# Optimization experiments

Hardware: AMD Instinct MI355X
Metric: run time of the kernel (lower is better)

Reference implementation:

```python
import jax, jax.numpy as jnp
import numpy as np

DIM = 768
H = 12
D = DIM // H            # 64
SCALE = D ** -0.5
M = 64                  # landmarks for pnp heads
PINV_ITERS = 6
PNP_HEADS = 11          # heads 0..10 use Nystrom, head 11 uses softmax


def setup_inputs() -> dict:
    key = jax.random.key(0)
    ks = jax.random.split(key, 5)
    B, N = 4, 4096
    x = jax.random.normal(ks[0], (B, N, DIM), jnp.float32)
    qkv_w = jax.random.normal(ks[1], (3 * DIM, DIM), jnp.float32) * (DIM ** -0.5)
    qkv_b = jax.random.normal(ks[2], (3 * DIM,), jnp.float32) * 0.01
    proj_w = jax.random.normal(ks[3], (DIM, DIM), jnp.float32) * (DIM ** -0.5)
    proj_b = jax.random.normal(ks[4], (DIM,), jnp.float32) * 0.01
    return {"x": x, "qkv_w": qkv_w, "qkv_b": qkv_b, "proj_w": proj_w, "proj_b": proj_b}


def moore_penrose_iter_pinv(x, iters=PINV_ITERS):
    # x: [B, h, M, M]. Original torch code takes torch.max over the whole per-head
    # tensor (incl. batch), so normalize with a per-head scalar over axes (B, M).
    abs_x = jnp.abs(x)
    col_max = abs_x.sum(axis=-1, keepdims=True).max(axis=(0, 2, 3), keepdims=True)
    row_max = abs_x.sum(axis=-2, keepdims=True).max(axis=(0, 2, 3), keepdims=True)
    z = jnp.swapaxes(x, -1, -2) / (col_max * row_max)
    I = jnp.eye(x.shape[-1], dtype=x.dtype)
    for _ in range(iters):
        xz = x @ z
        z = 0.25 * (z @ (13.0 * I - xz @ (15.0 * I - xz @ (7.0 * I - xz))))
    return z


def reference(x, qkv_w, qkv_b, proj_w, proj_b):
    B, N, C = x.shape
    qkv = (x @ qkv_w.T + qkv_b).reshape(B, N, 3, H, D).transpose(2, 0, 3, 1, 4)  # [3,B,H,N,D]
    q, k, v = qkv[0] * SCALE, qkv[1], qkv[2]

    # ---- Nystrom (pnp) heads 0..PNP_HEADS-1, all with the same M -> vectorized ----
    qp, kp, vp = q[:, :PNP_HEADS], k[:, :PNP_HEADS], v[:, :PNP_HEADS]
    idxs = jnp.array([int(i * N / M) for i in range(M)], dtype=jnp.int32)
    q_m = qp[:, :, idxs, :]   # [B,h,M,D] landmark queries
    k_m = kp[:, :, idxs, :]   # [B,h,M,D] landmark keys

    SA = jnp.einsum('bhnd,bhmd->bhnm', qp, k_m)   # [B,h,N,M]
    SC = jnp.einsum('bhmd,bhnd->bhmn', q_m, kp)   # [B,h,M,N]
    SB = jnp.einsum('bhmd,bhld->bhml', q_m, k_m)  # [B,h,M,M]

    eA = jnp.exp(SA - SA.max(axis=-1, keepdims=True))
    sc_max = SC.max(axis=-1, keepdims=True)       # [B,h,M,1]
    eC = jnp.exp(SC - sc_max)
    eB = jnp.exp(jnp.clip(SB - sc_max, -88.0, None))

    v_aug = jnp.concatenate([vp, jnp.ones_like(vp[..., :1])], axis=-1)  # [B,h,N,D+1]
    pi = moore_penrose_iter_pinv(eB)
    prod = (eA @ pi) @ (eC @ v_aug)               # [B,h,N,D+1]
    out_p = prod[..., :-1] / jnp.maximum(prod[..., -1:], 1e-8)

    # ---- fallback softmax head(s) ----
    qs, ks_, vs = q[:, PNP_HEADS:], k[:, PNP_HEADS:], v[:, PNP_HEADS:]
    attn = jax.nn.softmax(jnp.einsum('bhnd,bhmd->bhnm', qs, ks_), axis=-1)
    out_s = attn @ vs

    ctx = jnp.concatenate([out_p, out_s], axis=1).transpose(0, 2, 1, 3).reshape(B, N, C)
    return ctx @ proj_w.T + proj_b
```

## Files before the change

kernel.cpp:

```cpp
#include <hip/hip_runtime.h>


typedef __attribute__((ext_vector_type(8))) short short8;
typedef __attribute__((ext_vector_type(4))) float f32x4;
typedef __attribute__((ext_vector_type(4))) unsigned short ushort4v;

static __device__ __forceinline__ unsigned short f2bf(float f) {
    union { float f; unsigned u; } x; x.f = f;
    unsigned r = x.u + 0x7fffu + ((x.u >> 16) & 1u);
    return (unsigned short)(r >> 16);
}

static __device__ __forceinline__ float b2f(unsigned short u) {
    union { unsigned u; float f; } t; t.u = (unsigned)u << 16; return t.f;
}

static __device__ __forceinline__ void bfsplit(float x, unsigned short& h, unsigned short& l) {
    unsigned short hh = f2bf(x);
    union { unsigned u; float f; } t; t.u = (unsigned)hh << 16;
    h = hh;
    l = f2bf(x - t.f);
}

__global__ __launch_bounds__(256) void preconv(
    const float* __restrict__ in, unsigned short* __restrict__ hi,
    unsigned short* __restrict__ lo, int n4)
{
    for (int i = blockIdx.x * 256 + threadIdx.x; i < n4; i += gridDim.x * 256) {
        float4 f = *(const float4*)(in + (size_t)i * 4);
        float vs[4] = {f.x, f.y, f.z, f.w};
        ushort4v h, l;
        #pragma unroll
        for (int j = 0; j < 4; ++j) {
            unsigned short hh, ll;
            bfsplit(vs[j], hh, ll);
            h[j] = hh; l[j] = ll;
        }
        *(ushort4v*)(hi + (size_t)i * 4) = h;
        *(ushort4v*)(lo + (size_t)i * 4) = l;
    }
}

__global__ __launch_bounds__(256, 2) void gemm_qk_mfma(
    const unsigned short* __restrict__ Xh, const unsigned short* __restrict__ Xl,
    const unsigned short* __restrict__ Wh, const unsigned short* __restrict__ Wl,
    const float* __restrict__ bias,
    unsigned short* __restrict__ qh, unsigned short* __restrict__ ql,
    unsigned short* __restrict__ kh, unsigned short* __restrict__ kl)
{
    __shared__ unsigned short Ah[4096], Al[4096], Bh[4096], Bl[4096];
    const int tid = threadIdx.x;
    const int bid = blockIdx.x;
    const int swz = (bid & 7) * 192 + (bid >> 3);
    const int brow = (swz / 12) << 7, bcol = (swz % 12) << 7;
    const int ln = tid & 63, wv = tid >> 6;
    const int wr = (wv >> 1) << 6, wc = (wv & 1) << 6;
    const int srow = tid >> 1, sc = (tid & 1) << 1;
    const size_t ag = (size_t)(brow + srow) * 768 + (sc << 3);
    const size_t bg = (size_t)(bcol + srow) * 768 + (sc << 3);
    const int fr = ln & 15, fc = ln >> 4;
    const int i0 = srow * 32 + (((sc + 0) ^ (srow & 3)) << 3);
    const int i1 = srow * 32 + (((sc + 1) ^ (srow & 3)) << 3);

    f32x4 acc[4][4] = {};
    for (int k0 = 0; k0 < 768; k0 += 32) {
        short8 xh0 = *(const short8*)(Xh + ag + k0);
        short8 xh1 = *(const short8*)(Xh + ag + k0 + 8);
        short8 xl0 = *(const short8*)(Xl + ag + k0);
        short8 xl1 = *(const short8*)(Xl + ag + k0 + 8);
        short8 wh0 = *(const short8*)(Wh + bg + k0);
        short8 wh1 = *(const short8*)(Wh + bg + k0 + 8);
        short8 wl0 = *(const short8*)(Wl + bg + k0);
        short8 wl1 = *(const short8*)(Wl + bg + k0 + 8);
        __syncthreads();
        *(short8*)&Ah[i0] = xh0; *(short8*)&Ah[i1] = xh1;
        *(short8*)&Al[i0] = xl0; *(short8*)&Al[i1] = xl1;
        *(short8*)&Bh[i0] = wh0; *(short8*)&Bh[i1] = wh1;
        *(short8*)&Bl[i0] = wl0; *(short8*)&Bl[i1] = wl1;
        __syncthreads();
        short8 ah[4], al[4], bh[4], bl[4];
        #pragma unroll
        for (int i = 0; i < 4; ++i) {
            int ar = wr + (i << 4) + fr;
            int aidx = ar * 32 + ((fc ^ (ar & 3)) << 3);
            ah[i] = *(short8*)&Ah[aidx];
            al[i] = *(short8*)&Al[aidx];
            int br2 = wc + (i << 4) + fr;
            int bidx = br2 * 32 + ((fc ^ (br2 & 3)) << 3);
            bh[i] = *(short8*)&Bh[bidx];
            bl[i] = *(short8*)&Bl[bidx];
        }
        #pragma unroll
        for (int i = 0; i < 4; ++i)
            #pragma unroll
            for (int j = 0; j < 4; ++j) {
                acc[i][j] = __builtin_amdgcn_mfma_f32_16x16x32_bf16(ah[i], bh[j], acc[i][j], 0, 0, 0);
                acc[i][j] = __builtin_amdgcn_mfma_f32_16x16x32_bf16(ah[i], bl[j], acc[i][j], 0, 0, 0);
                acc[i][j] = __builtin_amdgcn_mfma_f32_16x16x32_bf16(al[i], bh[j], acc[i][j], 0, 0, 0);
            }
    }
    const int fg = ln >> 4;
    #pragma unroll
    for (int j = 0; j < 4; ++j) {
        int c = bcol + wc + (j << 4) + fr;
        float bb = bias[c];
        int isk = c >> 9 >= 1 ? (c >= 768) : 0;
        int rem = c - (c >= 768 ? 768 : 0);
        int h = rem >> 6, d = rem & 63;
        #pragma unroll
        for (int i = 0; i < 4; ++i)
            #pragma unroll
            for (int r = 0; r < 4; ++r) {
                int row = brow + wr + (i << 4) + (fg << 2) + r;
                int b = row >> 12, n = row & 4095;
                float val = acc[i][j][r] + bb;
                size_t idx = (((size_t)(b * 12 + h) << 12) + n) * 64 + d;
                unsigned short hh, ll;
                if (c < 768) {
                    bfsplit(val * 0.125f, hh, ll);
                    qh[idx] = hh; ql[idx] = ll;
                } else {
                    bfsplit(val, hh, ll);
                    kh[idx] = hh; kl[idx] = ll;
                }
            }
        (void)isk;
    }
}

__global__ __launch_bounds__(256, 2) void gemm_v_mfma(
    const unsigned short* __restrict__ Xh, const unsigned short* __restrict__ Wh,
    const float* __restrict__ bias, unsigned short* __restrict__ vh)
{
    __shared__ unsigned short Ah[4096], Bh[4096];
    const int tid = threadIdx.x;
    const int bid = blockIdx.x;
    const int swz = (bid & 7) * 96 + (bid >> 3);
    const int brow = (swz / 6) << 7, bcol = 1536 + ((swz % 6) << 7);
    const int ln = tid & 63, wv = tid >> 6;
    const int wr = (wv >> 1) << 6, wc = (wv & 1) << 6;
    const int srow = tid >> 1, sc = (tid & 1) << 1;
    const size_t ag = (size_t)(brow + srow) * 768 + (sc << 3);
    const size_t bg = (size_t)(bcol + srow) * 768 + (sc << 3);
    const int fr = ln & 15, fc = ln >> 4;
    const int i0 = srow * 32 + (((sc + 0) ^ (srow & 3)) << 3);
    const int i1 = srow * 32 + (((sc + 1) ^ (srow & 3)) << 3);

    f32x4 acc[4][4] = {};
    for (int k0 = 0; k0 < 768; k0 += 32) {
        short8 xh0 = *(const short8*)(Xh + ag + k0);
        short8 xh1 = *(const short8*)(Xh + ag + k0 + 8);
        short8 wh0 = *(const short8*)(Wh + bg + k0);
        short8 wh1 = *(const short8*)(Wh + bg + k0 + 8);
        __syncthreads();
        *(short8*)&Ah[i0] = xh0; *(short8*)&Ah[i1] = xh1;
        *(short8*)&Bh[i0] = wh0; *(short8*)&Bh[i1] = wh1;
        __syncthreads();
        short8 ah[4], bh[4];
        #pragma unroll
        for (int i = 0; i < 4; ++i) {
            int ar = wr + (i << 4) + fr;
            ah[i] = *(short8*)&Ah[ar * 32 + ((fc ^ (ar & 3)) << 3)];
            int br2 = wc + (i << 4) + fr;
            bh[i] = *(short8*)&Bh[br2 * 32 + ((fc ^ (br2 & 3)) << 3)];
        }
        #pragma unroll
        for (int i = 0; i < 4; ++i)
            #pragma unroll
            for (int j = 0; j < 4; ++j)
                acc[i][j] = __builtin_amdgcn_mfma_f32_16x16x32_bf16(ah[i], bh[j], acc[i][j], 0, 0, 0);
    }
    const int fg = ln >> 4;
    #pragma unroll
    for (int j = 0; j < 4; ++j) {
        int c = bcol + wc + (j << 4) + fr;
        float bb = bias[c];
        int rem = c - 1536;
        int h = rem >> 6, d = rem & 63;
        #pragma unroll
        for (int i = 0; i < 4; ++i)
            #pragma unroll
            for (int r = 0; r < 4; ++r) {
                int row = brow + wr + (i << 4) + (fg << 2) + r;
                int b = row >> 12, n = row & 4095;
                float val = acc[i][j][r] + bb;
                size_t idx = (((size_t)(b * 12 + h) << 12) + n) * 64 + d;
                vh[idx] = f2bf(val);
            }
    }
}

__global__ __launch_bounds__(256) void wflash(
    const unsigned short* __restrict__ qh, const unsigned short* __restrict__ ql,
    const unsigned short* __restrict__ khg, const unsigned short* __restrict__ klg,
    const unsigned short* __restrict__ vhg,
    float* __restrict__ wacc, float* __restrict__ wl, float* __restrict__ wm)
{
    int chunk = blockIdx.x;
    int bh = blockIdx.y;
    int b = bh / 11, h = bh - b * 11;
    size_t base = ((size_t)(b * 12 + h)) << 12;
    __shared__ unsigned short kh_s[64][72], kl_s[64][72];
    __shared__ unsigned short vth[64][72];
    __shared__ unsigned short ph[4][16][72], pl[4][16][72];
    int tid = threadIdx.x;
    int wv = tid >> 6, ln = tid & 63;
    int rr = tid >> 2, dg = (tid & 3) << 4;
    const int arow = (wv << 4) + (ln & 15);
    const int ak0 = (ln >> 4) << 3;
    const int rg = (ln >> 4) << 2;
    short8 aqh0, aql0, aqh1, aql1;
    {
        size_t off = ((base + ((size_t)arow << 6)) << 6) + ak0;
        aqh0 = *(const short8*)(qh + off);
        aqh1 = *(const short8*)(qh + off + 32);
        aql0 = *(const short8*)(ql + off);
        aql1 = *(const short8*)(ql + off + 32);
    }
    f32x4 o_acc[4] = {};
    float mr[4] = {-1e30f, -1e30f, -1e30f, -1e30f};
    float lr[4] = {};
    for (int t = 0; t < 8; ++t) {
        int n0 = (chunk << 9) + (t << 6);
        __syncthreads();
        {
            size_t off = ((base + n0 + rr) << 6) + dg;
            *(short8*)&kh_s[rr][dg]     = *(const short8*)(khg + off);
            *(short8*)&kh_s[rr][dg + 8] = *(const short8*)(khg + off + 8);
            *(short8*)&kl_s[rr][dg]     = *(const short8*)(klg + off);
            *(short8*)&kl_s[rr][dg + 8] = *(const short8*)(klg + off + 8);
            short8 v0 = *(const short8*)(vhg + off);
            short8 v1 = *(const short8*)(vhg + off + 8);
            #pragma unroll
            for (int i = 0; i < 8; ++i) {
                vth[dg + i][rr]     = (unsigned short)v0[i];
                vth[dg + 8 + i][rr] = (unsigned short)v1[i];
            }
        }
        __syncthreads();
        f32x4 s_acc[4];
        #pragma unroll
        for (int jb = 0; jb < 4; ++jb) {
            f32x4 z = {};
            const int brow2 = (jb << 4) + (ln & 15);
            short8 bh0 = *(short8*)&kh_s[brow2][ak0];
            short8 bh1 = *(short8*)&kh_s[brow2][ak0 + 32];
            short8 bl0 = *(short8*)&kl_s[brow2][ak0];
            short8 bl1 = *(short8*)&kl_s[brow2][ak0 + 32];
            z = __builtin_amdgcn_mfma_f32_16x16x32_bf16(aqh0, bh0, z, 0, 0, 0);
            z = __builtin_amdgcn_mfma_f32_16x16x32_bf16(aqh0, bl0, z, 0, 0, 0);
            z = __builtin_amdgcn_mfma_f32_16x16x32_bf16(aql0, bh0, z, 0, 0, 0);
            z = __builtin_amdgcn_mfma_f32_16x16x32_bf16(aqh1, bh1, z, 0, 0, 0);
            z = __builtin_amdgcn_mfma_f32_16x16x32_bf16(aqh1, bl1, z, 0, 0, 0);
            z = __builtin_amdgcn_mfma_f32_16x16x32_bf16(aql1, bh1, z, 0, 0, 0);
            s_acc[jb] = z;
        }
        float mx[4];
        #pragma unroll
        for (int r = 0; r < 4; ++r)
            mx[r] = fmaxf(fmaxf(s_acc[0][r], s_acc[1][r]),
                          fmaxf(s_acc[2][r], s_acc[3][r]));
        #pragma unroll
        for (int off2 = 1; off2 < 16; off2 <<= 1)
            #pragma unroll
            for (int r = 0; r < 4; ++r)
                mx[r] = fmaxf(mx[r], __shfl_xor(mx[r], off2, 64));
        float fac[4];
        #pragma unroll
        for (int r = 0; r < 4; ++r) {
            float mn = fmaxf(mr[r], mx[r]);
            fac[r] = expf(mr[r] - mn);
            mr[r] = mn;
        }
        float rs[4] = {};
        #pragma unroll
        for (int jb = 0; jb < 4; ++jb)
            #pragma unroll
            for (int r = 0; r < 4; ++r) {
                float p = expf(s_acc[jb][r] - mr[r]);
                rs[r] += p;
                unsigned short hh, ll;
                bfsplit(p, hh, ll);
                ph[wv][rg + r][(jb << 4) + (ln & 15)] = hh;
                pl[wv][rg + r][(jb << 4) + (ln & 15)] = ll;
            }
        #pragma unroll
        for (int off2 = 1; off2 < 16; off2 <<= 1)
            #pragma unroll
            for (int r = 0; r < 4; ++r)
                rs[r] += __shfl_xor(rs[r], off2, 64);
        #pragma unroll
        for (int r = 0; r < 4; ++r) lr[r] = lr[r] * fac[r] + rs[r];
        #pragma unroll
        for (int jb = 0; jb < 4; ++jb)
            #pragma unroll
            for (int r = 0; r < 4; ++r)
                o_acc[jb][r] *= fac[r];
        short8 pah0 = *(short8*)&ph[wv][ln & 15][ak0];
        short8 pah1 = *(short8*)&ph[wv][ln & 15][ak0 + 32];
        short8 pal0 = *(short8*)&pl[wv][ln & 15][ak0];
        short8 pal1 = *(short8*)&pl[wv][ln & 15][ak0 + 32];
        #pragma unroll
        for (int jb = 0; jb < 4; ++jb) {
            const int brow2 = (jb << 4) + (ln & 15);
            short8 bv0 = *(short8*)&vth[brow2][ak0];
            short8 bv1 = *(short8*)&vth[brow2][ak0 + 32];
            f32x4 o = o_acc[jb];
            o = __builtin_amdgcn_mfma_f32_16x16x32_bf16(pah0, bv0, o, 0, 0, 0);
            o = __builtin_amdgcn_mfma_f32_16x16x32_bf16(pal0, bv0, o, 0, 0, 0);
            o = __builtin_amdgcn_mfma_f32_16x16x32_bf16(pah1, bv1, o, 0, 0, 0);
            o = __builtin_amdgcn_mfma_f32_16x16x32_bf16(pal1, bv1, o, 0, 0, 0);
            o_acc[jb] = o;
        }
    }
    int cidx = (bh << 3) + chunk;
    #pragma unroll
    for (int jb = 0; jb < 4; ++jb)
        #pragma unroll
        for (int r = 0; r < 4; ++r) {
            int row = (wv << 4) + rg + r, col = (jb << 4) + (ln & 15);
            wacc[((size_t)cidx << 12) + ((size_t)row << 6) + col] = o_acc[jb][r];
        }
    if ((ln & 15) == 0)
        #pragma unroll
        for (int r = 0; r < 4; ++r) {
            int row = (wv << 4) + rg + r;
            wl[cidx * 64 + row] = lr[r];
            wm[cidx * 64 + row] = mr[r];
        }
}

__global__ __launch_bounds__(256) void wmerge(
    const float* __restrict__ wacc, const float* __restrict__ wl,
    const float* __restrict__ wm,
    float* __restrict__ Wb, float* __restrict__ scm)
{
    int bh = blockIdx.x;
    int tid = threadIdx.x;
    __shared__ float fcs[8][64];
    if (tid < 64) {
        float mx = -1e30f;
        #pragma unroll
        for (int c = 0; c < 8; ++c)
            mx = fmaxf(mx, wm[((bh << 3) + c) * 64 + tid]);
        scm[(bh << 6) + tid] = mx;
        #pragma unroll
        for (int c = 0; c < 8; ++c)
            fcs[c][tid] = expf(wm[((bh << 3) + c) * 64 + tid] - mx);
    }
    __syncthreads();
    for (int e = tid; e < 4096; e += 256) {
        int m = e >> 6, j = e & 63;
        float s = 0.f;
        #pragma unroll
        for (int c = 0; c < 8; ++c)
            s += fcs[c][m] * wacc[((size_t)((bh << 3) + c) << 12) + e];
        Wb[(size_t)bh * 4160 + m * 65 + j] = s;
    }
    if (tid < 64) {
        float s = 0.f;
        #pragma unroll
        for (int c = 0; c < 8; ++c)
            s += fcs[c][tid] * wl[((bh << 3) + c) * 64 + tid];
        Wb[(size_t)bh * 4160 + tid * 65 + 64] = s;
    }
}

__global__ __launch_bounds__(256) void eb_kernel(
    const unsigned short* __restrict__ qh, const unsigned short* __restrict__ ql,
    const unsigned short* __restrict__ kh, const unsigned short* __restrict__ kl,
    const float* __restrict__ scm, float* __restrict__ eB)
{
    int bh = blockIdx.x;
    int b = bh / 11, h = bh - b * 11;
    size_t base = ((size_t)(b * 12 + h)) << 12;
    __shared__ float qm[64][65], km[64][65];
    int tid = threadIdx.x;
    for (int e = tid; e < 4096; e += 256) {
        int mm = e >> 6, d = e & 63;
        size_t off = ((base + ((size_t)mm << 6)) << 6) + d;
        qm[mm][d] = b2f(qh[off]) + b2f(ql[off]);
        km[mm][d] = b2f(kh[off]) + b2f(kl[off]);
    }
    __syncthreads();
    int m = tid >> 2, l0 = tid & 3;
    float smax = scm[(bh << 6) + m];
    for (int l = l0; l < 64; l += 4) {
        float s = 0.f;
        #pragma unroll
        for (int d = 0; d < 64; ++d) s += qm[m][d] * km[l][d];
        eB[((size_t)bh << 12) + (m << 6) + l] = expf(fmaxf(s - smax, -88.f));
    }
}

__global__ __launch_bounds__(256) void norms_kernel(
    const float* __restrict__ eB, float* __restrict__ denom)
{
    int h = blockIdx.x;
    int tid = threadIdx.x;
    int b = tid >> 6, idx = tid & 63;
    int bh = b * 11 + h;
    const float* E = eB + ((size_t)bh << 12);
    float rs = 0.f, cs = 0.f;
    #pragma unroll 4
    for (int l = 0; l < 64; ++l) rs += E[(idx << 6) + l];
    #pragma unroll 4
    for (int m = 0; m < 64; ++m) cs += E[(m << 6) + idx];
    __shared__ float r1[256], r2[256];
    r1[tid] = rs; r2[tid] = cs;
    __syncthreads();
    for (int s = 128; s > 0; s >>= 1) {
        if (tid < s) {
            r1[tid] = fmaxf(r1[tid], r1[tid + s]);
            r2[tid] = fmaxf(r2[tid], r2[tid + s]);
        }
        __syncthreads();
    }
    if (tid == 0) denom[h] = r1[0] * r2[0];
}

__device__ __forceinline__ void mm64x3(
    const unsigned short (&Ahi)[64][72], const unsigned short (&Alo)[64][72],
    const unsigned short (&BThi)[64][72], const unsigned short (&BTlo)[64][72],
    int wr, int wc, int fr, int fk, f32x4 (&acc)[2][2])
{
    #pragma unroll
    for (int ks = 0; ks < 2; ++ks) {
        const int kb = (ks << 5) + fk;
        short8 ah[2], al[2], bh[2], bl[2];
        #pragma unroll
        for (int i = 0; i < 2; ++i) {
            ah[i] = *(const short8*)&Ahi[wr + (i << 4) + fr][kb];
            al[i] = *(const short8*)&Alo[wr + (i << 4) + fr][kb];
            bh[i] = *(const short8*)&BThi[wc + (i << 4) + fr][kb];
            bl[i] = *(const short8*)&BTlo[wc + (i << 4) + fr][kb];
        }
        #pragma unroll
        for (int i = 0; i < 2; ++i)
            #pragma unroll
            for (int j = 0; j < 2; ++j) {
                acc[i][j] = __builtin_amdgcn_mfma_f32_16x16x32_bf16(ah[i], bh[j], acc[i][j], 0, 0, 0);
                acc[i][j] = __builtin_amdgcn_mfma_f32_16x16x32_bf16(ah[i], bl[j], acc[i][j], 0, 0, 0);
                acc[i][j] = __builtin_amdgcn_mfma_f32_16x16x32_bf16(al[i], bh[j], acc[i][j], 0, 0, 0);
            }
    }
}

__global__ __launch_bounds__(256) void pinv_kernel(
    const float* __restrict__ eB, const float* __restrict__ denom,
    float* __restrict__ pi_)
{
    __shared__ unsigned short Xh[64][72],  Xl[64][72];
    __shared__ unsigned short Zh[64][72],  Zl[64][72];
    __shared__ unsigned short ZTh[64][72], ZTl[64][72];
    __shared__ unsigned short Mh[64][72],  Ml[64][72];
    __shared__ unsigned short MTh[64][72], MTl[64][72];
    __shared__ unsigned short Th[64][72],  Tbl[64][72];
    __shared__ float Zf[64][68];
    int bh = blockIdx.x;
    int h = bh % 11;
    int tid = threadIdx.x;
    float dn = denom[h];
    const int ln = tid & 63, wv = tid >> 6;
    const int wr = (wv >> 1) << 5, wc = (wv & 1) << 5;
    const int fr = ln & 15, fk = (ln >> 4) << 3;
    const int rg = (ln >> 4) << 2;

    for (int e = tid; e < 4096; e += 256) {
        int m = e >> 6, l = e & 63;
        float xv = eB[((size_t)bh << 12) + e];
        unsigned short hh, ll;
        bfsplit(xv, hh, ll);
        Xh[m][l] = hh; Xl[m][l] = ll;
        float zv = xv / dn;
        Zf[l][m] = zv;
        bfsplit(zv, hh, ll);
        Zh[l][m] = hh; Zl[l][m] = ll;
        ZTh[m][l] = hh; ZTl[m][l] = ll;
    }
    __syncthreads();

    for (int it = 0; it < 6; ++it) {
        f32x4 mm1[2][2] = {};
        mm64x3(Xh, Xl, ZTh, ZTl, wr, wc, fr, fk, mm1);
        #pragma unroll
        for (int i = 0; i < 2; ++i)
            #pragma unroll
            for (int j = 0; j < 2; ++j)
                #pragma unroll
                for (int r = 0; r < 4; ++r) {
                    int row = wr + (i << 4) + rg + r, col = wc + (j << 4) + fr;
                    unsigned short hh, ll;
                    bfsplit(mm1[i][j][r], hh, ll);
                    Mh[row][col] = hh;  Ml[row][col] = ll;
                    MTh[col][row] = hh; MTl[col][row] = ll;
                }
        __syncthreads();
        f32x4 a2[2][2] = {};
        mm64x3(Mh, Ml, MTh, MTl, wr, wc, fr, fk, a2);
        #pragma unroll
        for (int i = 0; i < 2; ++i)
            #pragma unroll
            for (int j = 0; j < 2; ++j)
                #pragma unroll
                for (int r = 0; r < 4; ++r) {
                    int row = wr + (i << 4) + rg + r, col = wc + (j << 4) + fr;
                    float val = 7.f * mm1[i][j][r] - a2[i][j][r];
                    unsigned short hh, ll;
                    bfsplit(val, hh, ll);
                    Th[col][row] = hh; Tbl[col][row] = ll;
                }
        __syncthreads();
        f32x4 a3[2][2] = {};
        mm64x3(Mh, Ml, Th, Tbl, wr, wc, fr, fk, a3);
        __syncthreads();
        #pragma unroll
        for (int i = 0; i < 2; ++i)
            #pragma unroll
            for (int j = 0; j < 2; ++j)
                #pragma unroll
                for (int r = 0; r < 4; ++r) {
                    int row = wr + (i << 4) + rg + r, col = wc + (j << 4) + fr;
                    float val = 15.f * mm1[i][j][r] - a3[i][j][r];
                    unsigned short hh, ll;
                    bfsplit(val, hh, ll);
                    Th[col][row] = hh; Tbl[col][row] = ll;
                }
        __syncthreads();
        f32x4 a4[2][2] = {};
        mm64x3(Zh, Zl, Th, Tbl, wr, wc, fr, fk, a4);
        float zn[2][2][4];
        #pragma unroll
        for (int i = 0; i < 2; ++i)
            #pragma unroll
            for (int j = 0; j < 2; ++j)
                #pragma unroll
                for (int r = 0; r < 4; ++r) {
                    int row = wr + (i << 4) + rg + r, col = wc + (j << 4) + fr;
                    zn[i][j][r] = 0.25f * (13.f * Zf[row][col] - a4[i][j][r]);
                }
        __syncthreads();
        #pragma unroll
        for (int i = 0; i < 2; ++i)
            #pragma unroll
            for (int j = 0; j < 2; ++j)
                #pragma unroll
                for (int r = 0; r < 4; ++r) {
                    int row = wr + (i << 4) + rg + r, col = wc + (j << 4) + fr;
                    float val = zn[i][j][r];
                    Zf[row][col] = val;
                    unsigned short hh, ll;
                    bfsplit(val, hh, ll);
                    Zh[row][col] = hh;  Zl[row][col] = ll;
                    ZTh[col][row] = hh; ZTl[col][row] = ll;
                }
        __syncthreads();
    }
    for (int e = tid; e < 4096; e += 256)
        pi_[((size_t)bh << 12) + e] = Zf[e >> 6][e & 63];
}

__global__ __launch_bounds__(256) void pw_kernel(
    const float* __restrict__ pi_, const float* __restrict__ Wb,
    float* __restrict__ Tb)
{
    int bh = blockIdx.x;
    __shared__ float P[64][65];
    __shared__ float Wl[64][66];
    int tid = threadIdx.x;
    for (int e = tid; e < 4096; e += 256)
        P[e >> 6][e & 63] = pi_[((size_t)bh << 12) + e];
    for (int e = tid; e < 64 * 65; e += 256) {
        int l = e / 65, j = e - l * 65;
        Wl[l][j] = Wb[(size_t)bh * 4160 + e];
    }
    __syncthreads();
    int m = tid & 63, g = tid >> 6;
    #pragma unroll
    for (int t = 0; t < 17; ++t) {
        int j = g + (t << 2);
        if (j > 64) break;
        float s = 0.f;
        #pragma unroll
        for (int l = 0; l < 64; ++l) s += P[m][l] * Wl[l][j];
        Tb[(size_t)((bh << 6) + m) * 65 + j] = s;
    }
}

__global__ __launch_bounds__(256) void outp_kernel(
    const unsigned short* __restrict__ qh, const unsigned short* __restrict__ ql,
    const unsigned short* __restrict__ khg, const unsigned short* __restrict__ klg,
    const float* __restrict__ Tb, unsigned short* __restrict__ ctxh)
{
    int bh = blockIdx.y;
    int b = bh / 11, h = bh - b * 11;
    int n0 = blockIdx.x << 6;
    size_t base = ((size_t)(b * 12 + h)) << 12;
    __shared__ unsigned short kmh[64][72], kml[64][72];
    __shared__ unsigned short tth[64][72], ttl[64][72];
    __shared__ unsigned short ph[4][16][72], pl[4][16][72];
    __shared__ float t64[64];
    int tid = threadIdx.x;
    int wv = tid >> 6, ln = tid & 63;
    int rr = tid >> 2, dg = (tid & 3) << 4;
    const int arow = (wv << 4) + (ln & 15);
    const int ak0 = (ln >> 4) << 3;
    const int rg = (ln >> 4) << 2;
    {
        size_t off = ((base + ((size_t)rr << 6)) << 6) + dg;
        *(short8*)&kmh[rr][dg]     = *(const short8*)(khg + off);
        *(short8*)&kmh[rr][dg + 8] = *(const short8*)(khg + off + 8);
        *(short8*)&kml[rr][dg]     = *(const short8*)(klg + off);
        *(short8*)&kml[rr][dg + 8] = *(const short8*)(klg + off + 8);
    }
    for (int e = tid; e < 4096; e += 256) {
        int m = e >> 6, j = e & 63;
        float tv = Tb[(size_t)((bh << 6) + m) * 65 + j];
        unsigned short hh, ll;
        bfsplit(tv, hh, ll);
        tth[j][m] = hh; ttl[j][m] = ll;
    }
    if (tid < 64) t64[tid] = Tb[(size_t)((bh << 6) + tid) * 65 + 64];
    short8 aqh0, aql0, aqh1, aql1;
    {
        size_t off = ((base + n0 + arow) << 6) + ak0;
        aqh0 = *(const short8*)(qh + off);
        aqh1 = *(const short8*)(qh + off + 32);
        aql0 = *(const short8*)(ql + off);
        aql1 = *(const short8*)(ql + off + 32);
    }
    __syncthreads();
    f32x4 s_acc[4];
    #pragma unroll
    for (int jb = 0; jb < 4; ++jb) {
        f32x4 z = {};
        const int brow2 = (jb << 4) + (ln & 15);
        short8 bh0 = *(short8*)&kmh[brow2][ak0];
        short8 bh1 = *(short8*)&kmh[brow2][ak0 + 32];
        short8 bl0 = *(short8*)&kml[brow2][ak0];
        short8 bl1 = *(short8*)&kml[brow2][ak0 + 32];
        z = __builtin_amdgcn_mfma_f32_16x16x32_bf16(aqh0, bh0, z, 0, 0, 0);
        z = __builtin_amdgcn_mfma_f32_16x16x32_bf16(aqh0, bl0, z, 0, 0, 0);
        z = __builtin_amdgcn_mfma_f32_16x16x32_bf16(aql0, bh0, z, 0, 0, 0);
        z = __builtin_amdgcn_mfma_f32_16x16x32_bf16(aqh1, bh1, z, 0, 0, 0);
        z = __builtin_amdgcn_mfma_f32_16x16x32_bf16(aqh1, bl1, z, 0, 0, 0);
        z = __builtin_amdgcn_mfma_f32_16x16x32_bf16(aql1, bh1, z, 0, 0, 0);
        s_acc[jb] = z;
    }
    float mx[4];
    #pragma unroll
    for (int r = 0; r < 4; ++r)
        mx[r] = fmaxf(fmaxf(s_acc[0][r], s_acc[1][r]),
                      fmaxf(s_acc[2][r], s_acc[3][r]));
    #pragma unroll
    for (int off2 = 1; off2 < 16; off2 <<= 1)
        #pragma unroll
        for (int r = 0; r < 4; ++r)
            mx[r] = fmaxf(mx[r], __shfl_xor(mx[r], off2, 64));
    float den[4] = {};
    #pragma unroll
    for (int jb = 0; jb < 4; ++jb) {
        float tj = t64[(jb << 4) + (ln & 15)];
        #pragma unroll
        for (int r = 0; r < 4; ++r) {
            float p = expf(s_acc[jb][r] - mx[r]);
            den[r] += p * tj;
            unsigned short hh, ll;
            bfsplit(p, hh, ll);
            ph[wv][rg + r][(jb << 4) + (ln & 15)] = hh;
            pl[wv][rg + r][(jb << 4) + (ln & 15)] = ll;
        }
    }
    #pragma unroll
    for (int off2 = 1; off2 < 16; off2 <<= 1)
        #pragma unroll
        for (int r = 0; r < 4; ++r)
            den[r] += __shfl_xor(den[r], off2, 64);
    short8 pah0 = *(short8*)&ph[wv][ln & 15][ak0];
    short8 pah1 = *(short8*)&ph[wv][ln & 15][ak0 + 32];
    short8 pal0 = *(short8*)&pl[wv][ln & 15][ak0];
    short8 pal1 = *(short8*)&pl[wv][ln & 15][ak0 + 32];
    f32x4 o_acc[4] = {};
    #pragma unroll
    for (int jb = 0; jb < 4; ++jb) {
        const int brow2 = (jb << 4) + (ln & 15);
        short8 bth0 = *(short8*)&tth[brow2][ak0];
        short8 bth1 = *(short8*)&tth[brow2][ak0 + 32];
        short8 btl0 = *(short8*)&ttl[brow2][ak0];
        short8 btl1 = *(short8*)&ttl[brow2][ak0 + 32];
        f32x4 o = o_acc[jb];
        o = __builtin_amdgcn_mfma_f32_16x16x32_bf16(pah0, bth0, o, 0, 0, 0);
        o = __builtin_amdgcn_mfma_f32_16x16x32_bf16(pah0, btl0, o, 0, 0, 0);
        o = __builtin_amdgcn_mfma_f32_16x16x32_bf16(pal0, bth0, o, 0, 0, 0);
        o = __builtin_amdgcn_mfma_f32_16x16x32_bf16(pah1, bth1, o, 0, 0, 0);
        o = __builtin_amdgcn_mfma_f32_16x16x32_bf16(pah1, btl1, o, 0, 0, 0);
        o = __builtin_amdgcn_mfma_f32_16x16x32_bf16(pal1, bth1, o, 0, 0, 0);
        o_acc[jb] = o;
    }
    float inv[4];
    #pragma unroll
    for (int r = 0; r < 4; ++r) inv[r] = 1.0f / fmaxf(den[r], 1e-8f);
    #pragma unroll
    for (int jb = 0; jb < 4; ++jb)
        #pragma unroll
        for (int r = 0; r < 4; ++r) {
            int row = n0 + (wv << 4) + rg + r;
            int col = (jb << 4) + (ln & 15);
            ctxh[((size_t)b * 4096 + row) * 768 + h * 64 + col] =
                f2bf(o_acc[jb][r] * inv[r]);
        }
}

__global__ __launch_bounds__(256) void flash_part(
    const unsigned short* __restrict__ qhg, const unsigned short* __restrict__ khg,
    const unsigned short* __restrict__ vhg,
    float* __restrict__ pacc, float* __restrict__ pm, float* __restrict__ pl)
{
    int bx = blockIdx.x, cy = blockIdx.y, b = blockIdx.z;
    int n0 = bx << 6;
    size_t base = ((size_t)(b * 12 + 11)) << 12;
    __shared__ unsigned short qs[64][72];
    __shared__ unsigned short ks[64][72];
    __shared__ unsigned short vts[64][72];
    __shared__ unsigned short ps[4][16][72];
    int tid = threadIdx.x;
    int wv = tid >> 6, ln = tid & 63;
    int rr = tid >> 2, dg = (tid & 3) << 4;
    {
        size_t off = ((base + n0 + rr) << 6) + dg;
        *(short8*)&qs[rr][dg]     = *(const short8*)(qhg + off);
        *(short8*)&qs[rr][dg + 8] = *(const short8*)(qhg + off + 8);
    }
    __syncthreads();
    const int arow = (wv << 4) + (ln & 15);
    const int ak0 = (ln >> 4) << 3;
    const int rg = (ln >> 4) << 2;
    short8 aq0 = *(short8*)&qs[arow][ak0];
    short8 aq1 = *(short8*)&qs[arow][ak0 + 32];
    f32x4 o_acc[4] = {};
    float mr[4] = {-1e30f, -1e30f, -1e30f, -1e30f};
    float lr[4] = {};
    for (int t = 0; t < 16; ++t) {
        int m0 = (cy << 10) + (t << 6);
        __syncthreads();
        {
            size_t off = ((base + m0 + rr) << 6) + dg;
            *(short8*)&ks[rr][dg]     = *(const short8*)(khg + off);
            *(short8*)&ks[rr][dg + 8] = *(const short8*)(khg + off + 8);
            short8 v0 = *(const short8*)(vhg + off);
            short8 v1 = *(const short8*)(vhg + off + 8);
            #pragma unroll
            for (int i = 0; i < 8; ++i) {
                vts[dg + i][rr]     = (unsigned short)v0[i];
                vts[dg + 8 + i][rr] = (unsigned short)v1[i];
            }
        }
        __syncthreads();
        f32x4 s_acc[4];
        #pragma unroll
        for (int jb = 0; jb < 4; ++jb) {
            f32x4 z = {};
            short8 bk0 = *(short8*)&ks[(jb << 4) + (ln & 15)][ak0];
            short8 bk1 = *(short8*)&ks[(jb << 4) + (ln & 15)][ak0 + 32];
            z = __builtin_amdgcn_mfma_f32_16x16x32_bf16(aq0, bk0, z, 0, 0, 0);
            z = __builtin_amdgcn_mfma_f32_16x16x32_bf16(aq1, bk1, z, 0, 0, 0);
            s_acc[jb] = z;
        }
        float mx[4];
        #pragma unroll
        for (int r = 0; r < 4; ++r)
            mx[r] = fmaxf(fmaxf(s_acc[0][r], s_acc[1][r]),
                          fmaxf(s_acc[2][r], s_acc[3][r]));
        #pragma unroll
        for (int off2 = 1; off2 < 16; off2 <<= 1)
            #pragma unroll
            for (int r = 0; r < 4; ++r)
                mx[r] = fmaxf(mx[r], __shfl_xor(mx[r], off2, 64));
        float fac[4];
        #pragma unroll
        for (int r = 0; r < 4; ++r) {
            float mn = fmaxf(mr[r], mx[r]);
            fac[r] = expf(mr[r] - mn);
            mr[r] = mn;
        }
        float rs[4] = {};
        #pragma unroll
        for (int jb = 0; jb < 4; ++jb)
            #pragma unroll
            for (int r = 0; r < 4; ++r) {
                float p = expf(s_acc[jb][r] - mr[r]);
                rs[r] += p;
                ps[wv][rg + r][(jb << 4) + (ln & 15)] = f2bf(p);
            }
        #pragma unroll
        for (int off2 = 1; off2 < 16; off2 <<= 1)
            #pragma unroll
            for (int r = 0; r < 4; ++r)
                rs[r] += __shfl_xor(rs[r], off2, 64);
        #pragma unroll
        for (int r = 0; r < 4; ++r) lr[r] = lr[r] * fac[r] + rs[r];
        #pragma unroll
        for (int jb = 0; jb < 4; ++jb)
            #pragma unroll
            for (int r = 0; r < 4; ++r)
                o_acc[jb][r] *= fac[r];
        short8 pa0 = *(short8*)&ps[wv][ln & 15][ak0];
        short8 pa1 = *(short8*)&ps[wv][ln & 15][ak0 + 32];
        #pragma unroll
        for (int jb = 0; jb < 4; ++jb) {
            short8 bv0 = *(short8*)&vts[(jb << 4) + (ln & 15)][ak0];
            short8 bv1 = *(short8*)&vts[(jb << 4) + (ln & 15)][ak0 + 32];
            f32x4 z = o_acc[jb];
            z = __builtin_amdgcn_mfma_f32_16x16x32_bf16(pa0, bv0, z, 0, 0, 0);
            z = __builtin_amdgcn_mfma_f32_16x16x32_bf16(pa1, bv1, z, 0, 0, 0);
            o_acc[jb] = z;
        }
    }
    int slot = (b * 4 + cy) * 64 + bx;
    #pragma unroll
    for (int jb = 0; jb < 4; ++jb)
        #pragma unroll
        for (int r = 0; r < 4; ++r) {
            int row = (wv << 4) + rg + r, col = (jb << 4) + (ln & 15);
            pacc[(size_t)slot * 4096 + (size_t)row * 64 + col] = o_acc[jb][r];
        }
    if ((ln & 15) == 0)
        #pragma unroll
        for (int r = 0; r < 4; ++r) {
            int row = (wv << 4) + rg + r;
            pm[(size_t)slot * 64 + row] = mr[r];
            pl[(size_t)slot * 64 + row] = lr[r];
        }
}

__global__ __launch_bounds__(256) void flash_merge(
    const float* __restrict__ pacc, const float* __restrict__ pm,
    const float* __restrict__ pl, unsigned short* __restrict__ ctxh)
{
    int bx = blockIdx.x, b = blockIdx.y;
    int tid = threadIdx.x, r = tid & 63, g = tid >> 6;
    float mc[4], mt = -1e30f;
    #pragma unroll
    for (int c = 0; c < 4; ++c) {
        mc[c] = pm[(size_t)((b * 4 + c) * 64 + bx) * 64 + r];
        mt = fmaxf(mt, mc[c]);
    }
    float fac[4], lt = 0.f;
    #pragma unroll
    for (int c = 0; c < 4; ++c) {
        fac[c] = expf(mc[c] - mt);
        lt += fac[c] * pl[(size_t)((b * 4 + c) * 64 + bx) * 64 + r];
    }
    float inv = 1.0f / lt;
    size_t obase = ((size_t)b * 4096 + (size_t)((bx << 6) + r)) * 768 + 11 * 64 + (g << 4);
    #pragma unroll
    for (int i = 0; i < 16; ++i) {
        float s = 0.f;
        #pragma unroll
        for (int c = 0; c < 4; ++c)
            s += fac[c] * pacc[(size_t)((b * 4 + c) * 64 + bx) * 4096 + (size_t)r * 64 + (g << 4) + i];
        ctxh[obase + i] = f2bf(s * inv);
    }
}

__global__ __launch_bounds__(256, 2) void gemm_proj_mfma(
    const unsigned short* __restrict__ Xh, const unsigned short* __restrict__ Wh,
    const float* __restrict__ bias, float* __restrict__ out)
{
    __shared__ unsigned short Ah[4096], Bh[4096];
    const int tid = threadIdx.x;
    const int bid = blockIdx.x;
    const int swz = (bid & 7) * 96 + (bid >> 3);
    const int brow = (swz / 6) << 7, bcol = (swz % 6) << 7;
    const int ln = tid & 63, wv = tid >> 6;
    const int wr = (wv >> 1) << 6, wc = (wv & 1) << 6;
    const int srow = tid >> 1, sc = (tid & 1) << 1;
    const size_t ag = (size_t)(brow + srow) * 768 + (sc << 3);
    const size_t bg = (size_t)(bcol + srow) * 768 + (sc << 3);
    const int fr = ln & 15, fc = ln >> 4;
    const int i0 = srow * 32 + (((sc + 0) ^ (srow & 3)) << 3);
    const int i1 = srow * 32 + (((sc + 1) ^ (srow & 3)) << 3);

    f32x4 acc[4][4] = {};
    for (int k0 = 0; k0 < 768; k0 += 32) {
        short8 xh0 = *(const short8*)(Xh + ag + k0);
        short8 xh1 = *(const short8*)(Xh + ag + k0 + 8);
        short8 wh0 = *(const short8*)(Wh + bg + k0);
        short8 wh1 = *(const short8*)(Wh + bg + k0 + 8);
        __syncthreads();
        *(short8*)&Ah[i0] = xh0; *(short8*)&Ah[i1] = xh1;
        *(short8*)&Bh[i0] = wh0; *(short8*)&Bh[i1] = wh1;
        __syncthreads();
        short8 ah[4], bh[4];
        #pragma unroll
        for (int i = 0; i < 4; ++i) {
            int ar = wr + (i << 4) + fr;
            ah[i] = *(short8*)&Ah[ar * 32 + ((fc ^ (ar & 3)) << 3)];
            int br2 = wc + (i << 4) + fr;
            bh[i] = *(short8*)&Bh[br2 * 32 + ((fc ^ (br2 & 3)) << 3)];
        }
        #pragma unroll
        for (int i = 0; i < 4; ++i)
            #pragma unroll
            for (int j = 0; j < 4; ++j)
                acc[i][j] = __builtin_amdgcn_mfma_f32_16x16x32_bf16(ah[i], bh[j], acc[i][j], 0, 0, 0);
    }
    const int fg = ln >> 4;
    #pragma unroll
    for (int j = 0; j < 4; ++j) {
        int c = bcol + wc + (j << 4) + fr;
        float bb = bias[c];
        #pragma unroll
        for (int i = 0; i < 4; ++i)
            #pragma unroll
            for (int r = 0; r < 4; ++r) {
                int row = brow + wr + (i << 4) + (fg << 2) + r;
                out[(size_t)row * 768 + c] = acc[i][j][r] + bb;
            }
    }
}

extern "C" void kernel_launch(void* const* d_in, const int* in_sizes, int n_in,
                              void* d_out, int out_size, void* d_ws, size_t ws_size,
                              hipStream_t stream)
{
    const float* x      = (const float*)d_in[0];
    const float* qkv_w  = (const float*)d_in[1];
    const float* qkv_b  = (const float*)d_in[2];
    const float* proj_w = (const float*)d_in[3];
    const float* proj_b = (const float*)d_in[4];
    float* out = (float*)d_out;

    const size_t QKV = (size_t)4 * 12 * 4096 * 64;
    unsigned short* qh = (unsigned short*)d_ws;
    unsigned short* ql = qh + QKV;
    unsigned short* kh = ql + QKV;
    unsigned short* kl = kh + QKV;
    unsigned short* vh = kl + QKV;
    unsigned short* ctxh = vh + QKV;
    float* scm  = (float*)(ctxh + QKV);
    float* eB   = scm + 4096;
    float* den  = eB + 44 * 4096;
    float* pi_  = den + 64;
    float* Wb   = pi_ + 44 * 4096;
    float* Tb   = Wb + 44 * 4160;
    unsigned short* Whi  = (unsigned short*)(Tb + 44 * 4160);
    unsigned short* Wlo  = Whi + (size_t)2304 * 768;
    unsigned short* Pwhi = Wlo + (size_t)2304 * 768;
    unsigned short* Pwlo = Pwhi + (size_t)768 * 768;

    unsigned short* Xhi = (unsigned short*)out;
    unsigned short* Xlo = Xhi + QKV;
    float* wacc = out;
    float* wl   = wacc + 1441792;
    float* wm   = wl + 22528;
    float* fpacc = out;
    float* fpm   = fpacc + 4194304;
    float* fpl   = fpm + 65536;

    preconv<<<2048, 256, 0, stream>>>(x, Xhi, Xlo, 3145728);
    preconv<<<1024, 256, 0, stream>>>(qkv_w, Whi, Wlo, 442368);
    preconv<<<512, 256, 0, stream>>>(proj_w, Pwhi, Pwlo, 147456);
    gemm_qk_mfma<<<1536, 256, 0, stream>>>(Xhi, Xlo, Whi, Wlo, qkv_b,
                                           qh, ql, kh, kl);
    gemm_v_mfma<<<768, 256, 0, stream>>>(Xhi, Whi, qkv_b, vh);
    wflash<<<dim3(8, 44), 256, 0, stream>>>(qh, ql, kh, kl, vh, wacc, wl, wm);
    wmerge<<<44, 256, 0, stream>>>(wacc, wl, wm, Wb, scm);
    eb_kernel<<<44, 256, 0, stream>>>(qh, ql, kh, kl, scm, eB);
    norms_kernel<<<11, 256, 0, stream>>>(eB, den);
    pinv_kernel<<<44, 256, 0, stream>>>(eB, den, pi_);
    pw_kernel<<<44, 256, 0, stream>>>(pi_, Wb, Tb);
    outp_kernel<<<dim3(64, 44), 256, 0, stream>>>(qh, ql, kh, kl, Tb, ctxh);
    flash_part<<<dim3(64, 4, 4), 256, 0, stream>>>(qh, kh, vh, fpacc, fpm, fpl);
    flash_merge<<<dim3(64, 4), 256, 0, stream>>>(fpacc, fpm, fpl, ctxh);
    gemm_proj_mfma<<<768, 256, 0, stream>>>(ctxh, Pwhi, proj_b, out);
}
```

Measured before the change: 456.3 us.

## Merge weight preconversion launches, deepen GEMM K-tiles, drop low-bf16 P terms

The three fp32-to-bf16 split launches become one kernel over a concatenated index range, which removes two launches. The V and projection GEMMs now stage 64-wide K tiles with an 8-way XOR swizzle, halving the number of barrier-separated iterations. The wflash and outp kernels no longer compute or use the low bf16 half of the softmax probabilities, which removes the shared-memory writes, loads and MFMAs for those terms. This lowers the precision of P in the Nystrom path, adding error that must stay within tolerance.

```diff
diff --git a/kernel.cpp b/kernel.cpp
--- a/kernel.cpp
+++ b/kernel.cpp
@@ -22,22 +22,31 @@
     l = f2bf(x - t.f);
 }
 
-__global__ __launch_bounds__(256) void preconv(
-    const float* __restrict__ in, unsigned short* __restrict__ hi,
-    unsigned short* __restrict__ lo, int n4)
-{
-    for (int i = blockIdx.x * 256 + threadIdx.x; i < n4; i += gridDim.x * 256) {
-        float4 f = *(const float4*)(in + (size_t)i * 4);
+__global__ __launch_bounds__(256) void preconv3(
+    const float* __restrict__ a, const float* __restrict__ b,
+    const float* __restrict__ c,
+    unsigned short* __restrict__ ahi, unsigned short* __restrict__ alo,
+    unsigned short* __restrict__ bhi, unsigned short* __restrict__ blo,
+    unsigned short* __restrict__ chi, unsigned short* __restrict__ clo)
+{
+    const int nA = 3145728, nB = 442368, nC = 147456;
+    const int total = nA + nB + nC;
+    for (int i = blockIdx.x * 256 + threadIdx.x; i < total; i += gridDim.x * 256) {
+        const float* src; unsigned short* hi; unsigned short* lo; int j;
+        if (i < nA)           { src = a; hi = ahi; lo = alo; j = i; }
+        else if (i < nA + nB) { src = b; hi = bhi; lo = blo; j = i - nA; }
+        else                  { src = c; hi = chi; lo = clo; j = i - nA - nB; }
+        float4 f = *(const float4*)(src + (size_t)j * 4);
         float vs[4] = {f.x, f.y, f.z, f.w};
         ushort4v h, l;
         #pragma unroll
-        for (int j = 0; j < 4; ++j) {
+        for (int t = 0; t < 4; ++t) {
             unsigned short hh, ll;
-            bfsplit(vs[j], hh, ll);
-            h[j] = hh; l[j] = ll;
-        }
-        *(ushort4v*)(hi + (size_t)i * 4) = h;
-        *(ushort4v*)(lo + (size_t)i * 4) = l;
+            bfsplit(vs[t], hh, ll);
+            h[t] = hh; l[t] = ll;
+        }
+        *(ushort4v*)(hi + (size_t)j * 4) = h;
+        *(ushort4v*)(lo + (size_t)j * 4) = l;
     }
 }
 
@@ -104,7 +113,6 @@
     for (int j = 0; j < 4; ++j) {
         int c = bcol + wc + (j << 4) + fr;
         float bb = bias[c];
-        int isk = c >> 9 >= 1 ? (c >= 768) : 0;
         int rem = c - (c >= 768 ? 768 : 0);
         int h = rem >> 6, d = rem & 63;
         #pragma unroll
@@ -124,7 +132,6 @@
                     kh[idx] = hh; kl[idx] = ll;
                 }
             }
-        (void)isk;
     }
 }
 
@@ -132,43 +139,52 @@
     const unsigned short* __restrict__ Xh, const unsigned short* __restrict__ Wh,
     const float* __restrict__ bias, unsigned short* __restrict__ vh)
 {
-    __shared__ unsigned short Ah[4096], Bh[4096];
+    __shared__ unsigned short Ah[8192], Bh[8192];
     const int tid = threadIdx.x;
     const int bid = blockIdx.x;
     const int swz = (bid & 7) * 96 + (bid >> 3);
     const int brow = (swz / 6) << 7, bcol = 1536 + ((swz % 6) << 7);
     const int ln = tid & 63, wv = tid >> 6;
     const int wr = (wv >> 1) << 6, wc = (wv & 1) << 6;
-    const int srow = tid >> 1, sc = (tid & 1) << 1;
-    const size_t ag = (size_t)(brow + srow) * 768 + (sc << 3);
-    const size_t bg = (size_t)(bcol + srow) * 768 + (sc << 3);
+    const int srow = tid >> 1;
+    const int c0 = (tid & 1) << 2;
+    const size_t ag = (size_t)(brow + srow) * 768;
+    const size_t bg = (size_t)(bcol + srow) * 768;
     const int fr = ln & 15, fc = ln >> 4;
-    const int i0 = srow * 32 + (((sc + 0) ^ (srow & 3)) << 3);
-    const int i1 = srow * 32 + (((sc + 1) ^ (srow & 3)) << 3);
 
     f32x4 acc[4][4] = {};
-    for (int k0 = 0; k0 < 768; k0 += 32) {
-        short8 xh0 = *(const short8*)(Xh + ag + k0);
-        short8 xh1 = *(const short8*)(Xh + ag + k0 + 8);
-        short8 wh0 = *(const short8*)(Wh + bg + k0);
-        short8 wh1 = *(const short8*)(Wh + bg + k0 + 8);
-        __syncthreads();
-        *(short8*)&Ah[i0] = xh0; *(short8*)&Ah[i1] = xh1;
-        *(short8*)&Bh[i0] = wh0; *(short8*)&Bh[i1] = wh1;
-        __syncthreads();
-        short8 ah[4], bh[4];
-        #pragma unroll
-        for (int i = 0; i < 4; ++i) {
-            int ar = wr + (i << 4) + fr;
-            ah[i] = *(short8*)&Ah[ar * 32 + ((fc ^ (ar & 3)) << 3)];
-            int br2 = wc + (i << 4) + fr;
-            bh[i] = *(short8*)&Bh[br2 * 32 + ((fc ^ (br2 & 3)) << 3)];
-        }
-        #pragma unroll
-        for (int i = 0; i < 4; ++i)
-            #pragma unroll
-            for (int j = 0; j < 4; ++j)
-                acc[i][j] = __builtin_amdgcn_mfma_f32_16x16x32_bf16(ah[i], bh[j], acc[i][j], 0, 0, 0);
+    for (int k0 = 0; k0 < 768; k0 += 64) {
+        short8 xa[4], wb[4];
+        #pragma unroll
+        for (int cc = 0; cc < 4; ++cc) {
+            xa[cc] = *(const short8*)(Xh + ag + k0 + ((c0 + cc) << 3));
+            wb[cc] = *(const short8*)(Wh + bg + k0 + ((c0 + cc) << 3));
+        }
+        __syncthreads();
+        #pragma unroll
+        for (int cc = 0; cc < 4; ++cc) {
+            int dst = srow * 64 + (((c0 + cc) ^ (srow & 7)) << 3);
+            *(short8*)&Ah[dst] = xa[cc];
+            *(short8*)&Bh[dst] = wb[cc];
+        }
+        __syncthreads();
+        #pragma unroll
+        for (int ks = 0; ks < 2; ++ks) {
+            const int kc = (ks << 2) + fc;
+            short8 ah[4], bh[4];
+            #pragma unroll
+            for (int i = 0; i < 4; ++i) {
+                int ar = wr + (i << 4) + fr;
+                ah[i] = *(short8*)&Ah[ar * 64 + ((kc ^ (ar & 7)) << 3)];
+                int br2 = wc + (i << 4) + fr;
+                bh[i] = *(short8*)&Bh[br2 * 64 + ((kc ^ (br2 & 7)) << 3)];
+            }
+            #pragma unroll
+            for (int i = 0; i < 4; ++i)
+                #pragma unroll
+                for (int j = 0; j < 4; ++j)
+                    acc[i][j] = __builtin_amdgcn_mfma_f32_16x16x32_bf16(ah[i], bh[j], acc[i][j], 0, 0, 0);
+        }
     }
     const int fg = ln >> 4;
     #pragma unroll
@@ -202,7 +218,7 @@
     size_t base = ((size_t)(b * 12 + h)) << 12;
     __shared__ unsigned short kh_s[64][72], kl_s[64][72];
     __shared__ unsigned short vth[64][72];
-    __shared__ unsigned short ph[4][16][72], pl[4][16][72];
+    __shared__ unsigned short ph[4][16][72];
     int tid = threadIdx.x;
     int wv = tid >> 6, ln = tid & 63;
     int rr = tid >> 2, dg = (tid & 3) << 4;
@@ -279,10 +295,7 @@
             for (int r = 0; r < 4; ++r) {
                 float p = expf(s_acc[jb][r] - mr[r]);
                 rs[r] += p;
-                unsigned short hh, ll;
-                bfsplit(p, hh, ll);
-                ph[wv][rg + r][(jb << 4) + (ln & 15)] = hh;
-                pl[wv][rg + r][(jb << 4) + (ln & 15)] = ll;
+                ph[wv][rg + r][(jb << 4) + (ln & 15)] = f2bf(p);
             }
         #pragma unroll
         for (int off2 = 1; off2 < 16; off2 <<= 1)
@@ -298,8 +311,6 @@
                 o_acc[jb][r] *= fac[r];
         short8 pah0 = *(short8*)&ph[wv][ln & 15][ak0];
         short8 pah1 = *(short8*)&ph[wv][ln & 15][ak0 + 32];
-        short8 pal0 = *(short8*)&pl[wv][ln & 15][ak0];
-        short8 pal1 = *(short8*)&pl[wv][ln & 15][ak0 + 32];
         #pragma unroll
         for (int jb = 0; jb < 4; ++jb) {
             const int brow2 = (jb << 4) + (ln & 15);
@@ -307,9 +318,7 @@
             short8 bv1 = *(short8*)&vth[brow2][ak0 + 32];
             f32x4 o = o_acc[jb];
             o = __builtin_amdgcn_mfma_f32_16x16x32_bf16(pah0, bv0, o, 0, 0, 0);
-            o = __builtin_amdgcn_mfma_f32_16x16x32_bf16(pal0, bv0, o, 0, 0, 0);
             o = __builtin_amdgcn_mfma_f32_16x16x32_bf16(pah1, bv1, o, 0, 0, 0);
-            o = __builtin_amdgcn_mfma_f32_16x16x32_bf16(pal1, bv1, o, 0, 0, 0);
             o_acc[jb] = o;
         }
     }
@@ -598,7 +607,7 @@
     size_t base = ((size_t)(b * 12 + h)) << 12;
     __shared__ unsigned short kmh[64][72], kml[64][72];
     __shared__ unsigned short tth[64][72], ttl[64][72];
-    __shared__ unsigned short ph[4][16][72], pl[4][16][72];
+    __shared__ unsigned short ph[4][16][72];
     __shared__ float t64[64];
     int tid = threadIdx.x;
     int wv = tid >> 6, ln = tid & 63;
@@ -665,10 +674,7 @@
         for (int r = 0; r < 4; ++r) {
             float p = expf(s_acc[jb][r] - mx[r]);
             den[r] += p * tj;
-            unsigned short hh, ll;
-            bfsplit(p, hh, ll);
-            ph[wv][rg + r][(jb << 4) + (ln & 15)] = hh;
-            pl[wv][rg + r][(jb << 4) + (ln & 15)] = ll;
+            ph[wv][rg + r][(jb << 4) + (ln & 15)] = f2bf(p);
         }
     }
     #pragma unroll
@@ -678,8 +684,6 @@
             den[r] += __shfl_xor(den[r], off2, 64);
     short8 pah0 = *(short8*)&ph[wv][ln & 15][ak0];
     short8 pah1 = *(short8*)&ph[wv][ln & 15][ak0 + 32];
-    short8 pal0 = *(short8*)&pl[wv][ln & 15][ak0];
-    short8 pal1 = *(short8*)&pl[wv][ln & 15][ak0 + 32];
     f32x4 o_acc[4] = {};
     #pragma unroll
     for (int jb = 0; jb < 4; ++jb) {
@@ -691,10 +695,8 @@
         f32x4 o = o_acc[jb];
         o = __builtin_amdgcn_mfma_f32_16x16x32_bf16(pah0, bth0, o, 0, 0, 0);
         o = __builtin_amdgcn_mfma_f32_16x16x32_bf16(pah0, btl0, o, 0, 0, 0);
-        o = __builtin_amdgcn_mfma_f32_16x16x32_bf16(pal0, bth0, o, 0, 0, 0);
         o = __builtin_amdgcn_mfma_f32_16x16x32_bf16(pah1, bth1, o, 0, 0, 0);
         o = __builtin_amdgcn_mfma_f32_16x16x32_bf16(pah1, btl1, o, 0, 0, 0);
-        o = __builtin_amdgcn_mfma_f32_16x16x32_bf16(pal1, bth1, o, 0, 0, 0);
         o_acc[jb] = o;
     }
     float inv[4];
@@ -867,43 +869,52 @@
     const unsigned short* __restrict__ Xh, const unsigned short* __restrict__ Wh,
     const float* __restrict__ bias, float* __restrict__ out)
 {
-    __shared__ unsigned short Ah[4096], Bh[4096];
+    __shared__ unsigned short Ah[8192], Bh[8192];
     const int tid = threadIdx.x;
     const int bid = blockIdx.x;
     const int swz = (bid & 7) * 96 + (bid >> 3);
     const int brow = (swz / 6) << 7, bcol = (swz % 6) << 7;
     const int ln = tid & 63, wv = tid >> 6;
     const int wr = (wv >> 1) << 6, wc = (wv & 1) << 6;
-    const int srow = tid >> 1, sc = (tid & 1) << 1;
-    const size_t ag = (size_t)(brow + srow) * 768 + (sc << 3);
-    const size_t bg = (size_t)(bcol + srow) * 768 + (sc << 3);
+    const int srow = tid >> 1;
+    const int c0 = (tid & 1) << 2;
+    const size_t ag = (size_t)(brow + srow) * 768;
+    const size_t bg = (size_t)(bcol + srow) * 768;
     const int fr = ln & 15, fc = ln >> 4;
-    const int i0 = srow * 32 + (((sc + 0) ^ (srow & 3)) << 3);
-    const int i1 = srow * 32 + (((sc + 1) ^ (srow & 3)) << 3);
 
     f32x4 acc[4][4] = {};
-    for (int k0 = 0; k0 < 768; k0 += 32) {
-        short8 xh0 = *(const short8*)(Xh + ag + k0);
-        short8 xh1 = *(const short8*)(Xh + ag + k0 + 8);
-        short8 wh0 = *(const short8*)(Wh + bg + k0);
-        short8 wh1 = *(const short8*)(Wh + bg + k0 + 8);
-        __syncthreads();
-        *(short8*)&Ah[i0] = xh0; *(short8*)&Ah[i1] = xh1;
-        *(short8*)&Bh[i0] = wh0; *(short8*)&Bh[i1] = wh1;
-        __syncthreads();
-        short8 ah[4], bh[4];
-        #pragma unroll
-        for (int i = 0; i < 4; ++i) {
-            int ar = wr + (i << 4) + fr;
-            ah[i] = *(short8*)&Ah[ar * 32 + ((fc ^ (ar & 3)) << 3)];
-            int br2 = wc + (i << 4) + fr;
-            bh[i] = *(short8*)&Bh[br2 * 32 + ((fc ^ (br2 & 3)) << 3)];
-        }
-        #pragma unroll
-        for (int i = 0; i < 4; ++i)
-            #pragma unroll
-            for (int j = 0; j < 4; ++j)
-                acc[i][j] = __builtin_amdgcn_mfma_f32_16x16x32_bf16(ah[i], bh[j], acc[i][j], 0, 0, 0);
+    for (int k0 = 0; k0 < 768; k0 += 64) {
+        short8 xa[4], wb[4];
+        #pragma unroll
+        for (int cc = 0; cc < 4; ++cc) {
+            xa[cc] = *(const short8*)(Xh + ag + k0 + ((c0 + cc) << 3));
+            wb[cc] = *(const short8*)(Wh + bg + k0 + ((c0 + cc) << 3));
+        }
+        __syncthreads();
+        #pragma unroll
+        for (int cc = 0; cc < 4; ++cc) {
+            int dst = srow * 64 + (((c0 + cc) ^ (srow & 7)) << 3);
+            *(short8*)&Ah[dst] = xa[cc];
+            *(short8*)&Bh[dst] = wb[cc];
+        }
+        __syncthreads();
+        #pragma unroll
+        for (int ks = 0; ks < 2; ++ks) {
+            const int kc = (ks << 2) + fc;
+            short8 ah[4], bh[4];
+            #pragma unroll
+            for (int i = 0; i < 4; ++i) {
+                int ar = wr + (i << 4) + fr;
+                ah[i] = *(short8*)&Ah[ar * 64 + ((kc ^ (ar & 7)) << 3)];
+                int br2 = wc + (i << 4) + fr;
+                bh[i] = *(short8*)&Bh[br2 * 64 + ((kc ^ (br2 & 7)) << 3)];
+            }
+            #pragma unroll
+            for (int i = 0; i < 4; ++i)
+                #pragma unroll
+                for (int j = 0; j < 4; ++j)
+                    acc[i][j] = __builtin_amdgcn_mfma_f32_16x16x32_bf16(ah[i], bh[j], acc[i][j], 0, 0, 0);
+        }
     }
     const int fg = ln >> 4;
     #pragma unroll
@@ -958,9 +969,8 @@
     float* fpm   = fpacc + 4194304;
     float* fpl   = fpm + 65536;
 
-    preconv<<<2048, 256, 0, stream>>>(x, Xhi, Xlo, 3145728);
-    preconv<<<1024, 256, 0, stream>>>(qkv_w, Whi, Wlo, 442368);
-    preconv<<<512, 256, 0, stream>>>(proj_w, Pwhi, Pwlo, 147456);
+    preconv3<<<2048, 256, 0, stream>>>(x, qkv_w, proj_w,
+                                       Xhi, Xlo, Whi, Wlo, Pwhi, Pwlo);
     gemm_qk_mfma<<<1536, 256, 0, stream>>>(Xhi, Xlo, Whi, Wlo, qkv_b,
                                            qh, ql, kh, kl);
     gemm_v_mfma<<<768, 256, 0, stream>>>(Xhi, Whi, qkv_b, vh);
```

Measured after the change: 436.9 us. 4.3% less time.
